# Performance work log

Measured on AMD Instinct MI355X. Metric: run time of the kernel, lower is better.

Reference implementation:

```python
import jax, jax.numpy as jnp
import numpy as np

BEAM = 10; MAX_LEN = 32; PAD = 1; BOS = 2; EOS = 3
NEG = jnp.float32(-1e30)


def lstm_cell(x, h, c, Wih, Whh, bih, bhh):
    # PyTorch LSTMCell gate order: i, f, g, o
    gates = x @ Wih.T + bih + h @ Whh.T + bhh
    i, f, g, o = jnp.split(gates, 4, axis=-1)
    c2 = jax.nn.sigmoid(f) * c + jax.nn.sigmoid(i) * jnp.tanh(g)
    h2 = jax.nn.sigmoid(o) * jnp.tanh(c2)
    return h2, c2


def setup_inputs() -> dict:
    key = jax.random.key(0)
    ks = jax.random.split(key, 14)
    G, P, E, H, S = 1000, 50000, 500, 500, 32
    s = lambda k, shape: jax.random.normal(k, shape, jnp.float32) * 0.05
    return {
        "g_seq": jax.random.randint(ks[0], (S, 1), 0, G),
        "enc_emb": s(ks[1], (G, E)),
        "enc_Wih": s(ks[2], (4 * H, E)), "enc_Whh": s(ks[3], (4 * H, H)),
        "enc_bih": s(ks[4], (4 * H,)), "enc_bhh": s(ks[5], (4 * H,)),
        "dec_emb": s(ks[6], (P, E)),
        "dec_Wih": s(ks[7], (4 * H, E)), "dec_Whh": s(ks[8], (4 * H, H)),
        "dec_bih": s(ks[9], (4 * H,)), "dec_bhh": s(ks[10], (4 * H,)),
        "attn_W": s(ks[11], (H, 2 * H)),
        "out_W": s(ks[12], (P, H)),
        "out_b": s(ks[13], (P,)),
    }


def reference(g_seq, enc_emb, enc_Wih, enc_Whh, enc_bih, enc_bhh,
              dec_emb, dec_Wih, dec_Whh, dec_bih, dec_bhh,
              attn_W, out_W, out_b):
    S = g_seq.shape[0]
    H = enc_Whh.shape[1]
    P = out_W.shape[0]

    # ---- encoder: unidirectional LSTMCell over seq, batch = 1 ----
    e_seq = enc_emb[g_seq[:, 0]]  # (S, E)
    def enc_step(carry, e):
        h, c = carry
        h, c = lstm_cell(e[None, :], h, c, enc_Wih, enc_Whh, enc_bih, enc_bhh)
        return (h, c), h[0]
    h0 = jnp.zeros((1, H), jnp.float32)
    (h, c), outs = jax.lax.scan(enc_step, (h0, h0), e_seq)  # outs: (S, H)

    # expand encoder state / context to beam
    context = jnp.broadcast_to(outs[None, :, :], (BEAM, S, H))
    h = jnp.broadcast_to(h, (BEAM, H))
    c = jnp.broadcast_to(c, (BEAM, H))
    scores = jnp.zeros((BEAM,), jnp.float32)
    tokens = jnp.full((BEAM,), PAD, jnp.int32).at[0].set(BOS)
    row0 = (jnp.arange(BEAM)[:, None] == 0)  # first-step mask: only beam 0 valid

    # ---- beam-search decode loop (run full max_len; early-eos break omitted,
    #      see notes: with eos=3 it only changes output when eos tops beam 0) ----
    def dec_step(carry, t):
        h, c, scores, tokens = carry
        e = dec_emb[tokens]                                   # (BEAM, E)
        h2, c2 = lstm_cell(e, h, c, dec_Wih, dec_Whh, dec_bih, dec_bhh)
        # dot attention
        attn = jax.nn.softmax(jnp.einsum('bsh,bh->bs', context, h2), axis=1)
        wctx = jnp.einsum('bs,bsh->bh', attn, context)
        o = jnp.tanh(jnp.concatenate([h2, wctx], axis=1) @ attn_W.T)
        logp = jax.nn.log_softmax(o @ out_W.T + out_b, axis=1)  # (BEAM, P)
        # first step: only beam 0 participates (original uses workd_lk[0])
        beam_lk = jnp.where(t == 0,
                            jnp.where(row0, logp, NEG),
                            logp + scores[:, None])
        best, idx = jax.lax.top_k(beam_lk.reshape(-1), BEAM)
        prev_k = idx // P
        next_y = idx - prev_k * P
        return (h2[prev_k], c2[prev_k], best, next_y), (prev_k, next_y)

    (_, _, scores, _), (prevKs, nextYs) = jax.lax.scan(
        dec_step, (h, c, scores, tokens), jnp.arange(MAX_LEN))

    # ---- hypothesis traceback, vectorized over beams ----
    def tb_step(k, t):
        tok = nextYs[t][k]
        return prevKs[t][k], tok
    _, toks = jax.lax.scan(tb_step, jnp.arange(BEAM), jnp.arange(MAX_LEN - 1, -1, -1))
    hyps = toks[::-1].T  # (BEAM, MAX_LEN)
    return hyps
```

## Files before the change

kernel.cpp:

```cpp
#include <hip/hip_runtime.h>
#include <math.h>

#define BEAM   10
#define MAXLEN 32
#define SLEN   32
#define HD     500
#define ED     500
#define G4     2000
#define PV     50000
#define NEGF   (-1e30f)

#define OFF_X      0
#define OFF_CBUF   64000
#define OFF_GBUF   65000
#define OFF_CTX    69000
#define OFF_DH     85000
#define OFF_DC     90000
#define OFF_DG     95000
#define OFF_H2     115000
#define OFF_C2     120000
#define OFF_O      130000
#define OFF_SCD    135000
#define OFF_TOK    135020
#define OFF_PREVK  135040
#define OFF_NEXTY  135360
#define OFF_PARTD  136000
#define OFF_CAND   152000
#define OFF_LOG    160000
#define OFF_OWT    660000
#define NEED_T_BYTES ((size_t)(OFF_OWT + (size_t)HD * PV) * 4)

typedef unsigned long long u64;

__device__ __forceinline__ float sigf(float x) { return 1.f / (1.f + expf(-x)); }

__device__ __forceinline__ unsigned fkey(float f) {
    unsigned u = __float_as_uint(f);
    return (u & 0x80000000u) ? ~u : (u | 0x80000000u);
}
__device__ __forceinline__ float unfkey(unsigned k) {
    unsigned u = (k & 0x80000000u) ? (k & 0x7fffffffu) : ~k;
    return __uint_as_float(u);
}

__global__ void k_prep(const int* __restrict__ g_seq, const float* __restrict__ enc_emb,
                       const float* __restrict__ Wih, const float* __restrict__ bih,
                       const float* __restrict__ bhh, float* __restrict__ X,
                       float* __restrict__ cbuf0) {
    if (blockIdx.x == 0) {
        for (int j = threadIdx.x; j < HD; j += 256) cbuf0[j] = 0.f;
    }
    int wv = (blockIdx.x * blockDim.x + threadIdx.x) >> 6;
    int lane = threadIdx.x & 63;
    if (wv >= SLEN * G4) return;
    int t = wv / G4, r = wv - t * G4;
    const float* emb = enc_emb + (size_t)g_seq[t] * ED;
    const float* w = Wih + (size_t)r * ED;
    float acc = 0.f;
    for (int ki = 0; ki < 8; ki++) { int k = ki * 64 + lane; if (k < ED) acc += emb[k] * w[k]; }
    for (int o = 32; o; o >>= 1) acc += __shfl_down(acc, o);
    if (lane == 0) X[t * G4 + r] = acc + bih[r] + bhh[r];
}

__global__ void k_transpose4(const float* __restrict__ outW, float* __restrict__ outW4) {
    __shared__ float t_lds[64][65];
    int tid = threadIdx.x;
    int pbase = blockIdx.x * 64, kbase = blockIdx.y * 64;
    for (int e = 0; e < 16; e++) {
        int idx = e * 256 + tid; int pl = idx >> 6, kl = idx & 63;
        int pp = pbase + pl, kk = kbase + kl;
        t_lds[pl][kl] = (pp < PV && kk < HD) ? outW[(size_t)pp * HD + kk] : 0.f;
    }
    __syncthreads();
    for (int e = 0; e < 4; e++) {
        int idx = e * 256 + tid;
        int pl = idx & 63, kb = idx >> 6;
        int pp = pbase + pl;
        int kglob = kbase + kb * 4;
        if (pp < PV && kglob < HD) {
            float4 v;
            v.x = t_lds[pl][kb * 4 + 0];
            v.y = t_lds[pl][kb * 4 + 1];
            v.z = t_lds[pl][kb * 4 + 2];
            v.w = t_lds[pl][kb * 4 + 3];
            *(float4*)(outW4 + ((size_t)(kbase / 4 + kb) * PV + pp) * 4) = v;
        }
    }
}

__global__ void k_enc(const float* __restrict__ Whh, const float* __restrict__ X,
                      float* __restrict__ gbuf, float* __restrict__ cbuf,
                      float* __restrict__ context, float* __restrict__ dec_h,
                      float* __restrict__ dec_c, double* __restrict__ scores,
                      int* __restrict__ tokens, int t) {
    __shared__ float h_lds[HD];
    const float* gprev = gbuf + ((t + 1) & 1) * G4;
    float*       gcur  = gbuf + (t & 1) * G4;
    const float* cprev = cbuf + ((t + 1) & 1) * HD;
    float*       ccur  = cbuf + (t & 1) * HD;
    int tid = threadIdx.x;
    if (t > 0) {
        for (int j = tid; j < HD; j += 256) {
            float gi = gprev[j], gf = gprev[HD + j], gg = gprev[2 * HD + j], go = gprev[3 * HD + j];
            float c = sigf(gf) * cprev[j] + sigf(gi) * tanhf(gg);
            float h = sigf(go) * tanhf(c);
            h_lds[j] = h;
            if (blockIdx.x == 0) {
                ccur[j] = c;
                context[(t - 1) * HD + j] = h;
                if (t == SLEN) {
                    for (int b = 0; b < BEAM; b++) { dec_h[b * HD + j] = h; dec_c[b * HD + j] = c; }
                }
            }
        }
    } else {
        for (int j = tid; j < HD; j += 256) h_lds[j] = 0.f;
    }
    if (t == SLEN && blockIdx.x == 0 && tid == 0) {
        for (int b = 0; b < BEAM; b++) scores[b] = 0.0;
        tokens[0] = 2; for (int b = 1; b < BEAM; b++) tokens[b] = 1;
    }
    __syncthreads();
    if (t < SLEN) {
        int wv = blockIdx.x * 4 + (tid >> 6), lane = tid & 63;
        for (int r = wv; r < G4; r += 1000) {
            const float* w = Whh + (size_t)r * HD;
            float acc = 0.f;
            for (int ki = 0; ki < 8; ki++) { int k = ki * 64 + lane; if (k < HD) acc += h_lds[k] * w[k]; }
            for (int o = 32; o; o >>= 1) acc += __shfl_down(acc, o);
            if (lane == 0) gcur[r] = X[t * G4 + r] + acc;
        }
    }
}

__global__ __launch_bounds__(1024) void k_gates(
        const float* __restrict__ dec_emb, const float* __restrict__ Wih,
        const float* __restrict__ Whh, const float* __restrict__ bih,
        const float* __restrict__ bhh, const int* __restrict__ tokens,
        const float* __restrict__ h_ws, float* __restrict__ gates) {
    __shared__ float e_lds[BEAM * ED];
    __shared__ float h_lds[BEAM * HD];
    int tid = threadIdx.x;
    for (int idx = tid; idx < BEAM * ED; idx += 1024) {
        int b = idx / ED, k = idx - b * ED;
        e_lds[idx] = dec_emb[(size_t)tokens[b] * ED + k];
        h_lds[idx] = h_ws[idx];
    }
    __syncthreads();
    int wv = tid >> 6, lane = tid & 63;
    int r = blockIdx.x * 16 + wv;
    const float* wi = Wih + (size_t)r * ED;
    const float* wh = Whh + (size_t)r * HD;
    float acc[BEAM];
#pragma unroll
    for (int b = 0; b < BEAM; b++) acc[b] = 0.f;
    for (int ki = 0; ki < 8; ki++) {
        int k = ki * 64 + lane;
        if (k < ED) {
            float w = wi[k];
#pragma unroll
            for (int b = 0; b < BEAM; b++) acc[b] += w * e_lds[b * ED + k];
        }
    }
    for (int ki = 0; ki < 8; ki++) {
        int k = ki * 64 + lane;
        if (k < HD) {
            float w = wh[k];
#pragma unroll
            for (int b = 0; b < BEAM; b++) acc[b] += w * h_lds[b * HD + k];
        }
    }
#pragma unroll
    for (int b = 0; b < BEAM; b++) {
        float v = acc[b];
        for (int o = 32; o; o >>= 1) v += __shfl_down(v, o);
        acc[b] = v;
    }
    if (lane == 0) {
        float bb = bih[r] + bhh[r];
#pragma unroll
        for (int b = 0; b < BEAM; b++) gates[b * G4 + r] = acc[b] + bb;
    }
}

__global__ __launch_bounds__(256) void k_attn_oproj(
        const float* __restrict__ gates, const float* __restrict__ c_ws,
        const float* __restrict__ context, const float* __restrict__ attnW,
        float* __restrict__ h2_ws, float* __restrict__ c2_ws, float* __restrict__ o_ws) {
    __shared__ float h2_lds[BEAM * HD];
    __shared__ float wctx_lds[BEAM * HD];
    __shared__ float s_lds[BEAM * SLEN];
    __shared__ float a_lds[BEAM * SLEN];
    int tid = threadIdx.x;
    int wv = tid >> 6, lane = tid & 63;
    for (int idx = tid; idx < BEAM * HD; idx += 256) {
        int b = idx / HD, j = idx - b * HD;
        float gi = gates[b * G4 + j], gf = gates[b * G4 + HD + j];
        float gg = gates[b * G4 + 2 * HD + j], go = gates[b * G4 + 3 * HD + j];
        float c = sigf(gf) * c_ws[idx] + sigf(gi) * tanhf(gg);
        float h2 = sigf(go) * tanhf(c);
        h2_lds[idx] = h2;
        if (blockIdx.x == 0) { c2_ws[idx] = c; h2_ws[idx] = h2; }
    }
    __syncthreads();
    for (int si = 0; si < 8; ++si) {
        int s = wv + 4 * si;
        float acc[BEAM];
#pragma unroll
        for (int b = 0; b < BEAM; b++) acc[b] = 0.f;
        for (int ki = 0; ki < 8; ki++) {
            int k = ki * 64 + lane;
            if (k < HD) {
                float c = context[s * HD + k];
#pragma unroll
                for (int b = 0; b < BEAM; b++) acc[b] += c * h2_lds[b * HD + k];
            }
        }
#pragma unroll
        for (int b = 0; b < BEAM; b++) {
            float v = acc[b];
            for (int o = 32; o; o >>= 1) v += __shfl_down(v, o);
            if (lane == 0) s_lds[b * SLEN + s] = v;
        }
    }
    __syncthreads();
    if (wv == 0) {
        for (int b = 0; b < BEAM; ++b) {
            float v = (lane < SLEN) ? s_lds[b * SLEN + lane] : -INFINITY;
            float m = v;
            for (int o = 32; o; o >>= 1) m = fmaxf(m, __shfl_xor(m, o));
            float e = (lane < SLEN) ? expf(v - m) : 0.f;
            float sum = e;
            for (int o = 32; o; o >>= 1) sum += __shfl_xor(sum, o);
            if (lane < SLEN) a_lds[b * SLEN + lane] = e / sum;
        }
    }
    __syncthreads();
    {
        float w0[BEAM], w1[BEAM];
#pragma unroll
        for (int b = 0; b < BEAM; b++) { w0[b] = 0.f; w1[b] = 0.f; }
        int j0 = tid, j1 = tid + 256;
        for (int s = 0; s < SLEN; ++s) {
            float c0 = (j0 < HD) ? context[s * HD + j0] : 0.f;
            float c1 = (j1 < HD) ? context[s * HD + j1] : 0.f;
#pragma unroll
            for (int b = 0; b < BEAM; b++) {
                float a = a_lds[b * SLEN + s];
                w0[b] += a * c0; w1[b] += a * c1;
            }
        }
#pragma unroll
        for (int b = 0; b < BEAM; b++) {
            if (j0 < HD) wctx_lds[b * HD + j0] = w0[b];
            if (j1 < HD) wctx_lds[b * HD + j1] = w1[b];
        }
    }
    __syncthreads();
    int j = blockIdx.x * 4 + wv;
    const float* w = attnW + (size_t)j * 1000;
    float acc[BEAM];
#pragma unroll
    for (int b = 0; b < BEAM; b++) acc[b] = 0.f;
    for (int ki = 0; ki < 16; ki++) {
        int k = ki * 64 + lane;
        if (k < 1000) {
            float wk = w[k];
#pragma unroll
            for (int b = 0; b < BEAM; b++) {
                float h = (k < HD) ? h2_lds[b * HD + k] : wctx_lds[b * HD + k - HD];
                acc[b] += wk * h;
            }
        }
    }
#pragma unroll
    for (int b = 0; b < BEAM; b++) {
        float v = acc[b];
        for (int o = 32; o; o >>= 1) v += __shfl_down(v, o);
        acc[b] = v;
    }
    if (lane == 0) {
#pragma unroll
        for (int b = 0; b < BEAM; b++) o_ws[b * HD + j] = tanhf(acc[b]);
    }
}

__global__ __launch_bounds__(256) void k_logits4(
        const float* __restrict__ outW4, const float* __restrict__ outB,
        const float* __restrict__ o_ws, float* __restrict__ logits,
        double* __restrict__ partials) {
    __shared__ __align__(16) float4 o4[BEAM * 125];
    __shared__ float part[4][64][BEAM];
    int tid = threadIdx.x;
    for (int idx = tid; idx < BEAM * 125; idx += 256) {
        int b = idx / 125, kb = idx - b * 125;
        o4[idx] = *(const float4*)(o_ws + b * HD + kb * 4);
    }
    __syncthreads();
    int kc = tid >> 6, pl = tid & 63;
    int p = blockIdx.x * 64 + pl;
    int pc = (p < PV) ? p : (PV - 1);
    int kb0 = kc * 32, kb1 = (kc == 3) ? 125 : (kb0 + 32);
    float acc[BEAM];
#pragma unroll
    for (int b = 0; b < BEAM; b++) acc[b] = 0.f;
    const float4* wp = (const float4*)outW4;
    for (int kb = kb0; kb < kb1; ++kb) {
        float4 w = wp[(size_t)kb * PV + pc];
#pragma unroll
        for (int b = 0; b < BEAM; b++) {
            float4 o = o4[b * 125 + kb];
            acc[b] += w.x * o.x + w.y * o.y + w.z * o.z + w.w * o.w;
        }
    }
#pragma unroll
    for (int b = 0; b < BEAM; b++) part[kc][pl][b] = acc[b];
    __syncthreads();
    if (tid < 64) {
        int p2 = blockIdx.x * 64 + tid;
        bool valid = (p2 < PV);
        float ob = outB[valid ? p2 : 0];
        double es[BEAM];
#pragma unroll
        for (int b = 0; b < BEAM; b++) {
            float lg = part[0][tid][b] + part[1][tid][b] + part[2][tid][b] + part[3][tid][b] + ob;
            if (valid) logits[(size_t)b * PV + p2] = lg;
            es[b] = valid ? exp((double)lg) : 0.0;
        }
#pragma unroll
        for (int b = 0; b < BEAM; b++) {
            for (int o = 32; o; o >>= 1) es[b] += __shfl_down(es[b], o);
        }
        if (tid == 0) {
#pragma unroll
            for (int b = 0; b < BEAM; b++) partials[blockIdx.x * BEAM + b] = es[b];
        }
    }
}

__global__ void k_logits_f(const float* __restrict__ outW, const float* __restrict__ outB,
                           const float* __restrict__ o_ws, float* __restrict__ logits,
                           double* __restrict__ partials) {
    __shared__ float o_lds[BEAM * HD];
    __shared__ double ered[4][BEAM];
    int tid = threadIdx.x;
    for (int idx = tid; idx < BEAM * HD; idx += 256) o_lds[idx] = o_ws[idx];
    __syncthreads();
    int wv = tid >> 6, lane = tid & 63;
    int w = blockIdx.x * 4 + wv;
    double esum = 0.0;
    for (int pi = 0; pi < 16; pi++) {
        int p = w * 16 + pi;
        if (p >= PV) break;
        const float* wr = outW + (size_t)p * HD;
        float acc[BEAM];
#pragma unroll
        for (int b = 0; b < BEAM; b++) acc[b] = 0.f;
        for (int ki = 0; ki < 8; ki++) {
            int k = ki * 64 + lane;
            if (k < HD) {
                float x = wr[k];
#pragma unroll
                for (int b = 0; b < BEAM; b++) acc[b] += x * o_lds[b * HD + k];
            }
        }
#pragma unroll
        for (int b = 0; b < BEAM; b++)
            for (int o = 32; o; o >>= 1) acc[b] += __shfl_xor(acc[b], o);
        if (lane < BEAM) {
            float lg = 0.f;
#pragma unroll
            for (int b = 0; b < BEAM; b++) if (lane == b) lg = acc[b];
            lg += outB[p];
            logits[(size_t)lane * PV + p] = lg;
            esum += exp((double)lg);
        }
    }
    if (lane < BEAM) ered[wv][lane] = esum;
    __syncthreads();
    if (tid < BEAM) partials[blockIdx.x * BEAM + tid] =
        ered[0][tid] + ered[1][tid] + ered[2][tid] + ered[3][tid];
}

__global__ __launch_bounds__(256) void k_topk_row(const float* __restrict__ logits,
                                                  u64* __restrict__ cands) {
    const int CH = 1563;
    int r = blockIdx.x >> 5, ci = blockIdx.x & 31;
    int base = ci * CH;
    int tid = threadIdx.x;
    int wv = tid >> 6, lane = tid & 63;
    u64 key[7];
#pragma unroll
    for (int e = 0; e < 7; e++) {
        int p = base + e * 256 + tid;
        key[e] = 0ull;
        if (p < base + CH && p < PV) {
            float v = logits[(size_t)r * PV + p];
            key[e] = ((u64)fkey(v) << 32) | (unsigned)(~(unsigned)p);
        }
    }
    __shared__ u64 wred[4];
    __shared__ u64 winlds;
    for (int round = 0; round < BEAM; round++) {
        u64 mx = 0ull;
#pragma unroll
        for (int e = 0; e < 7; e++) if (key[e] > mx) mx = key[e];
        for (int o = 32; o; o >>= 1) {
            u64 other = __shfl_down(mx, o);
            if (other > mx) mx = other;
        }
        if (lane == 0) wred[wv] = mx;
        __syncthreads();
        if (tid == 0) {
            u64 wn = wred[0];
            for (int i = 1; i < 4; i++) if (wred[i] > wn) wn = wred[i];
            winlds = wn;
            cands[blockIdx.x * BEAM + round] = wn;
        }
        __syncthreads();
        u64 win = winlds;
#pragma unroll
        for (int e = 0; e < 7; e++) if (key[e] == win) key[e] = 0ull;
    }
}

__global__ __launch_bounds__(256) void k_merge(
        const double* __restrict__ partials, int npart,
        const u64* __restrict__ cands,
        double* __restrict__ scores, int* __restrict__ tokens,
        const float* __restrict__ h2_ws, const float* __restrict__ c2_ws,
        float* __restrict__ h_ws, float* __restrict__ c_ws,
        int* __restrict__ prevKs, int* __restrict__ nextYs, int t) {
    __shared__ double wredd[4];
    __shared__ double lse_lds[BEAM];
    __shared__ double sc_lds[BEAM];
    __shared__ double bwv[4];
    __shared__ unsigned bwf[4];
    __shared__ double winv_s;
    __shared__ unsigned winf_s;
    __shared__ int pk_lds[BEAM];
    __shared__ int ny_lds[BEAM];
    __shared__ double val_lds[BEAM];
    int tid = threadIdx.x;
    int wv = tid >> 6, lane = tid & 63;
    if (tid < BEAM) sc_lds[tid] = scores[tid];
    for (int b = 0; b < BEAM; b++) {
        double s = 0.0;
        for (int j = tid; j < npart; j += 256) s += partials[j * BEAM + b];
        for (int o = 32; o; o >>= 1) s += __shfl_down(s, o);
        if (lane == 0) wredd[wv] = s;
        __syncthreads();
        if (tid == 0) lse_lds[b] = log(wredd[0] + wredd[1] + wredd[2] + wredd[3]);
        __syncthreads();
    }
    double   cv[13];
    unsigned cf[13];
#pragma unroll
    for (int e = 0; e < 13; e++) {
        int c = e * 256 + tid;
        cv[e] = -1.0e308; cf[e] = 0xFFFFFFFFu;
        if (c < 3200) {
            u64 k0 = cands[c];
            if (k0) {
                int r = c / 320;
                float v = unfkey((unsigned)(k0 >> 32));
                unsigned p = ~((unsigned)k0);
                double v2;
                if (t == 0) v2 = (r == 0) ? ((double)v - lse_lds[0]) : (double)NEGF;
                else        v2 = ((double)v - lse_lds[r]) + sc_lds[r];
                cv[e] = v2;
                cf[e] = (unsigned)r * PV + p;
            }
        }
    }
    for (int round = 0; round < BEAM; round++) {
        double bv = -1.0e308; unsigned bf = 0xFFFFFFFFu;
#pragma unroll
        for (int e = 0; e < 13; e++) {
            if (cv[e] > bv || (cv[e] == bv && cf[e] < bf)) { bv = cv[e]; bf = cf[e]; }
        }
        for (int o = 32; o; o >>= 1) {
            double ov = __shfl_down(bv, o);
            unsigned of = __shfl_down(bf, o);
            if (ov > bv || (ov == bv && of < bf)) { bv = ov; bf = of; }
        }
        if (lane == 0) { bwv[wv] = bv; bwf[wv] = bf; }
        __syncthreads();
        if (tid == 0) {
            double xv = bwv[0]; unsigned xf = bwf[0];
            for (int i = 1; i < 4; i++) {
                if (bwv[i] > xv || (bwv[i] == xv && bwf[i] < xf)) { xv = bwv[i]; xf = bwf[i]; }
            }
            winv_s = xv; winf_s = xf;
            int pk = (int)(xf / PV);
            int ny = (int)(xf - (unsigned)pk * PV);
            pk_lds[round] = pk; ny_lds[round] = ny; val_lds[round] = xv;
        }
        __syncthreads();
        unsigned wff = winf_s;
#pragma unroll
        for (int e = 0; e < 13; e++) {
            if (cf[e] == wff) { cv[e] = -1.0e308; cf[e] = 0xFFFFFFFFu; }
        }
    }
    if (tid < BEAM) {
        scores[tid] = val_lds[tid];
        tokens[tid] = ny_lds[tid];
        prevKs[t * BEAM + tid] = pk_lds[tid];
        nextYs[t * BEAM + tid] = ny_lds[tid];
    }
    __syncthreads();
    for (int idx = tid; idx < BEAM * HD; idx += 256) {
        int i = idx / HD, j = idx - i * HD;
        h_ws[idx] = h2_ws[pk_lds[i] * HD + j];
        c_ws[idx] = c2_ws[pk_lds[i] * HD + j];
    }
}

__global__ void k_traceback(const int* __restrict__ prevKs, const int* __restrict__ nextYs,
                            int* __restrict__ out) {
    int k = threadIdx.x;
    if (k >= BEAM) return;
    int cur = k;
    for (int t = MAXLEN - 1; t >= 0; t--) {
        out[k * MAXLEN + t] = nextYs[t * BEAM + cur];
        cur = prevKs[t * BEAM + cur];
    }
}

extern "C" void kernel_launch(void* const* d_in, const int* in_sizes, int n_in,
                              void* d_out, int out_size, void* d_ws, size_t ws_size,
                              hipStream_t stream) {
    const int*   g_seq  = (const int*)  d_in[0];
    const float* encEmb = (const float*)d_in[1];
    const float* encWih = (const float*)d_in[2];
    const float* encWhh = (const float*)d_in[3];
    const float* encBih = (const float*)d_in[4];
    const float* encBhh = (const float*)d_in[5];
    const float* decEmb = (const float*)d_in[6];
    const float* decWih = (const float*)d_in[7];
    const float* decWhh = (const float*)d_in[8];
    const float* decBih = (const float*)d_in[9];
    const float* decBhh = (const float*)d_in[10];
    const float* attnW  = (const float*)d_in[11];
    const float* outW   = (const float*)d_in[12];
    const float* outB   = (const float*)d_in[13];

    float* ws = (float*)d_ws;
    float*  X     = ws + OFF_X;
    float*  cbuf  = ws + OFF_CBUF;
    float*  gbuf  = ws + OFF_GBUF;
    float*  ctx   = ws + OFF_CTX;
    float*  dh    = ws + OFF_DH;
    float*  dc    = ws + OFF_DC;
    float*  dg    = ws + OFF_DG;
    float*  h2    = ws + OFF_H2;
    float*  c2    = ws + OFF_C2;
    float*  o     = ws + OFF_O;
    double* sc    = (double*)(ws + OFF_SCD);
    int*    tok   = (int*)(ws + OFF_TOK);
    int*    prevK = (int*)(ws + OFF_PREVK);
    int*    nextY = (int*)(ws + OFF_NEXTY);
    double* part  = (double*)(ws + OFF_PARTD);
    u64*    cand  = (u64*)(ws + OFF_CAND);
    float*  logits = ws + OFF_LOG;
    float*  outW4  = ws + OFF_OWT;

    bool bigws = (ws_size >= NEED_T_BYTES);

    k_prep<<<16000, 256, 0, stream>>>(g_seq, encEmb, encWih, encBih, encBhh, X, cbuf);
    if (bigws) k_transpose4<<<dim3(782, 8), 256, 0, stream>>>(outW, outW4);

    for (int t = 0; t <= SLEN; t++)
        k_enc<<<250, 256, 0, stream>>>(encWhh, X, gbuf, cbuf, ctx, dh, dc, sc, tok, t);

    const int npart = 782;
    for (int t = 0; t < MAXLEN; t++) {
        k_gates<<<125, 1024, 0, stream>>>(decEmb, decWih, decWhh, decBih, decBhh, tok, dh, dg);
        k_attn_oproj<<<125, 256, 0, stream>>>(dg, dc, ctx, attnW, h2, c2, o);
        if (bigws) k_logits4<<<782, 256, 0, stream>>>(outW4, outB, o, logits, part);
        else       k_logits_f<<<782, 256, 0, stream>>>(outW, outB, o, logits, part);
        k_topk_row<<<320, 256, 0, stream>>>(logits, cand);
        k_merge<<<1, 256, 0, stream>>>(part, npart, cand, sc, tok, h2, c2, dh, dc, prevK, nextY, t);
    }
    k_traceback<<<1, 64, 0, stream>>>(prevK, nextY, (int*)d_out);
}
```

Before: 4.218 ms.

## Fuse encoder and beam-search decode loop into one cooperative persistent kernel

New measurement: 4.217 ms. No clear change (-0.0%).

```diff
diff --git a/kernel.cpp b/kernel.cpp
--- a/kernel.cpp
+++ b/kernel.cpp
@@ -1,5 +1,8 @@
 #include <hip/hip_runtime.h>
+#include <hip/hip_cooperative_groups.h>
 #include <math.h>
+
+namespace cg = cooperative_groups;
 
 #define BEAM   10
 #define MAXLEN 32
@@ -9,6 +12,13 @@
 #define G4     2000
 #define PV     50000
 #define NEGF   (-1e30f)
+
+#define GRID   256
+#define NW     1024
+
+#define NCHUNK 25
+#define CHSZ   2000
+#define CANDN  (NCHUNK * BEAM * BEAM)
 
 #define OFF_X      0
 #define OFF_CBUF   64000
@@ -84,6 +94,445 @@
             v.z = t_lds[pl][kb * 4 + 2];
             v.w = t_lds[pl][kb * 4 + 3];
             *(float4*)(outW4 + ((size_t)(kbase / 4 + kb) * PV + pp) * 4) = v;
+        }
+    }
+}
+
+struct MegaA {
+    const float* encWhh; const float* X;
+    float* gbuf; float* cbuf; float* ctx;
+    const float* decEmb; const float* decWih; const float* decWhh;
+    const float* decBih; const float* decBhh; const float* attnW;
+    const float* outW4; const float* outW; const float* outB;
+    float* dh; float* dc; float* dg; float* h2w; float* c2w; float* ow;
+    float* logits; double* sc; double* part;
+    int* tok; int* prevK; int* nextY; u64* cand; int* outTok;
+    int bigws; int npart;
+};
+
+struct TopkSm { u64 wred[4]; u64 win; };
+struct MergeSm {
+    double wredd[4];
+    double lse[BEAM];
+    double scl[BEAM];
+    double bwv[4];
+    unsigned bwf[4];
+    unsigned winf;
+    int pk[BEAM]; int ny[BEAM];
+    double val[BEAM];
+};
+
+__global__ __launch_bounds__(256) void k_mega(MegaA A) {
+    __shared__ __align__(16) char smem_raw[43584];
+    float* smf = (float*)smem_raw;
+    cg::grid_group grid = cg::this_grid();
+    const int tid = threadIdx.x, bid = blockIdx.x;
+    const int wv = tid >> 6, lane = tid & 63;
+    const int gw = bid * 4 + wv;
+
+    for (int t = 0; t <= SLEN; ++t) {
+        const float* gprev = A.gbuf + ((t + 1) & 1) * G4;
+        float*       gcur  = A.gbuf + (t & 1) * G4;
+        const float* cprev = A.cbuf + ((t + 1) & 1) * HD;
+        float*       ccur  = A.cbuf + (t & 1) * HD;
+        bool par = (t < SLEN) || (bid == 0);
+        if (par) {
+            float* h_lds = smf;
+            if (t > 0) {
+                for (int j = tid; j < HD; j += 256) {
+                    float gi = gprev[j], gf = gprev[HD + j], gg = gprev[2 * HD + j], go = gprev[3 * HD + j];
+                    float c = sigf(gf) * cprev[j] + sigf(gi) * tanhf(gg);
+                    float h = sigf(go) * tanhf(c);
+                    h_lds[j] = h;
+                    if (bid == 0) {
+                        ccur[j] = c;
+                        A.ctx[(t - 1) * HD + j] = h;
+                        if (t == SLEN) {
+                            for (int b = 0; b < BEAM; b++) { A.dh[b * HD + j] = h; A.dc[b * HD + j] = c; }
+                        }
+                    }
+                }
+            } else {
+                for (int j = tid; j < HD; j += 256) h_lds[j] = 0.f;
+            }
+            if (t == SLEN && bid == 0 && tid == 0) {
+                for (int b = 0; b < BEAM; b++) A.sc[b] = 0.0;
+                A.tok[0] = 2; for (int b = 1; b < BEAM; b++) A.tok[b] = 1;
+            }
+            __syncthreads();
+            if (t < SLEN) {
+                for (int r = gw; r < G4; r += NW) {
+                    const float* w = A.encWhh + (size_t)r * HD;
+                    float acc = 0.f;
+                    for (int ki = 0; ki < 8; ki++) { int k = ki * 64 + lane; if (k < HD) acc += h_lds[k] * w[k]; }
+                    for (int o = 32; o; o >>= 1) acc += __shfl_down(acc, o);
+                    if (lane == 0) gcur[r] = A.X[t * G4 + r] + acc;
+                }
+            }
+        }
+        grid.sync();
+    }
+
+    for (int t = 0; t < MAXLEN; ++t) {
+        {
+            float* e_lds = smf;
+            float* h_lds = smf + BEAM * ED;
+            for (int idx = tid; idx < BEAM * ED; idx += 256) {
+                int b = idx / ED, k = idx - b * ED;
+                e_lds[idx] = A.decEmb[(size_t)A.tok[b] * ED + k];
+                h_lds[idx] = A.dh[idx];
+            }
+            __syncthreads();
+            for (int r = gw; r < G4; r += NW) {
+                const float* wi = A.decWih + (size_t)r * ED;
+                const float* wh = A.decWhh + (size_t)r * HD;
+                float acc[BEAM];
+#pragma unroll
+                for (int b = 0; b < BEAM; b++) acc[b] = 0.f;
+                for (int ki = 0; ki < 8; ki++) {
+                    int k = ki * 64 + lane;
+                    if (k < ED) {
+                        float w = wi[k];
+#pragma unroll
+                        for (int b = 0; b < BEAM; b++) acc[b] += w * e_lds[b * ED + k];
+                    }
+                }
+                for (int ki = 0; ki < 8; ki++) {
+                    int k = ki * 64 + lane;
+                    if (k < HD) {
+                        float w = wh[k];
+#pragma unroll
+                        for (int b = 0; b < BEAM; b++) acc[b] += w * h_lds[b * HD + k];
+                    }
+                }
+#pragma unroll
+                for (int b = 0; b < BEAM; b++) {
+                    float v = acc[b];
+                    for (int o = 32; o; o >>= 1) v += __shfl_down(v, o);
+                    acc[b] = v;
+                }
+                if (lane == 0) {
+                    float bb = A.decBih[r] + A.decBhh[r];
+#pragma unroll
+                    for (int b = 0; b < BEAM; b++) A.dg[b * G4 + r] = acc[b] + bb;
+                }
+            }
+        }
+        grid.sync();
+
+        if (bid < 125) {
+            float* h2_lds   = smf;
+            float* wctx_lds = smf + 5000;
+            float* s_lds    = smf + 10000;
+            float* a_lds    = smf + 10320;
+            for (int idx = tid; idx < BEAM * HD; idx += 256) {
+                int b = idx / HD, j = idx - b * HD;
+                float gi = A.dg[b * G4 + j], gf = A.dg[b * G4 + HD + j];
+                float gg = A.dg[b * G4 + 2 * HD + j], go = A.dg[b * G4 + 3 * HD + j];
+                float c = sigf(gf) * A.dc[idx] + sigf(gi) * tanhf(gg);
+                float h2 = sigf(go) * tanhf(c);
+                h2_lds[idx] = h2;
+                if (bid == 0) { A.c2w[idx] = c; A.h2w[idx] = h2; }
+            }
+            __syncthreads();
+            for (int si = 0; si < 8; ++si) {
+                int s = wv + 4 * si;
+                float acc[BEAM];
+#pragma unroll
+                for (int b = 0; b < BEAM; b++) acc[b] = 0.f;
+                for (int ki = 0; ki < 8; ki++) {
+                    int k = ki * 64 + lane;
+                    if (k < HD) {
+                        float c = A.ctx[s * HD + k];
+#pragma unroll
+                        for (int b = 0; b < BEAM; b++) acc[b] += c * h2_lds[b * HD + k];
+                    }
+                }
+#pragma unroll
+                for (int b = 0; b < BEAM; b++) {
+                    float v = acc[b];
+                    for (int o = 32; o; o >>= 1) v += __shfl_down(v, o);
+                    if (lane == 0) s_lds[b * SLEN + s] = v;
+                }
+            }
+            __syncthreads();
+            if (wv == 0) {
+                for (int b = 0; b < BEAM; ++b) {
+                    float v = (lane < SLEN) ? s_lds[b * SLEN + lane] : -INFINITY;
+                    float m = v;
+                    for (int o = 32; o; o >>= 1) m = fmaxf(m, __shfl_xor(m, o));
+                    float e = (lane < SLEN) ? expf(v - m) : 0.f;
+                    float sum = e;
+                    for (int o = 32; o; o >>= 1) sum += __shfl_xor(sum, o);
+                    if (lane < SLEN) a_lds[b * SLEN + lane] = e / sum;
+                }
+            }
+            __syncthreads();
+            {
+                float w0[BEAM], w1[BEAM];
+#pragma unroll
+                for (int b = 0; b < BEAM; b++) { w0[b] = 0.f; w1[b] = 0.f; }
+                int j0 = tid, j1 = tid + 256;
+                for (int s = 0; s < SLEN; ++s) {
+                    float c0 = (j0 < HD) ? A.ctx[s * HD + j0] : 0.f;
+                    float c1 = (j1 < HD) ? A.ctx[s * HD + j1] : 0.f;
+#pragma unroll
+                    for (int b = 0; b < BEAM; b++) {
+                        float a = a_lds[b * SLEN + s];
+                        w0[b] += a * c0; w1[b] += a * c1;
+                    }
+                }
+#pragma unroll
+                for (int b = 0; b < BEAM; b++) {
+                    if (j0 < HD) wctx_lds[b * HD + j0] = w0[b];
+                    if (j1 < HD) wctx_lds[b * HD + j1] = w1[b];
+                }
+            }
+            __syncthreads();
+            int j = gw;
+            const float* w = A.attnW + (size_t)j * 1000;
+            float acc[BEAM];
+#pragma unroll
+            for (int b = 0; b < BEAM; b++) acc[b] = 0.f;
+            for (int ki = 0; ki < 16; ki++) {
+                int k = ki * 64 + lane;
+                if (k < 1000) {
+                    float wk = w[k];
+#pragma unroll
+                    for (int b = 0; b < BEAM; b++) {
+                        float h = (k < HD) ? h2_lds[b * HD + k] : wctx_lds[b * HD + k - HD];
+                        acc[b] += wk * h;
+                    }
+                }
+            }
+#pragma unroll
+            for (int b = 0; b < BEAM; b++) {
+                float v = acc[b];
+                for (int o = 32; o; o >>= 1) v += __shfl_down(v, o);
+                acc[b] = v;
+            }
+            if (lane == 0) {
+#pragma unroll
+                for (int b = 0; b < BEAM; b++) A.ow[b * HD + j] = tanhf(acc[b]);
+            }
+        }
+        grid.sync();
+
+        {
+            float4* o4 = (float4*)smem_raw;
+            for (int idx = tid; idx < BEAM * 125; idx += 256) {
+                int b = idx / 125, kb = idx - b * 125;
+                o4[idx] = *(const float4*)(A.ow + b * HD + kb * 4);
+            }
+            __syncthreads();
+            if (A.bigws) {
+                float* partl = (float*)(smem_raw + 20032);
+                for (int pt = bid; pt < 782; pt += GRID) {
+                    int kc = tid >> 6, pl = tid & 63;
+                    int p = pt * 64 + pl;
+                    int pc = (p < PV) ? p : (PV - 1);
+                    int kb0 = kc * 32, kb1 = (kc == 3) ? 125 : (kb0 + 32);
+                    float acc[BEAM];
+#pragma unroll
+                    for (int b = 0; b < BEAM; b++) acc[b] = 0.f;
+                    const float4* wp = (const float4*)A.outW4;
+                    for (int kb = kb0; kb < kb1; ++kb) {
+                        float4 w = wp[(size_t)kb * PV + pc];
+#pragma unroll
+                        for (int b = 0; b < BEAM; b++) {
+                            float4 o = o4[b * 125 + kb];
+                            acc[b] += w.x * o.x + w.y * o.y + w.z * o.z + w.w * o.w;
+                        }
+                    }
+#pragma unroll
+                    for (int b = 0; b < BEAM; b++) partl[(kc * 64 + pl) * BEAM + b] = acc[b];
+                    __syncthreads();
+                    if (tid < 64) {
+                        int p2 = pt * 64 + tid;
+                        bool valid = (p2 < PV);
+                        float ob = A.outB[valid ? p2 : 0];
+                        double es[BEAM];
+#pragma unroll
+                        for (int b = 0; b < BEAM; b++) {
+                            float lg = partl[(0 * 64 + tid) * BEAM + b] + partl[(1 * 64 + tid) * BEAM + b]
+                                     + partl[(2 * 64 + tid) * BEAM + b] + partl[(3 * 64 + tid) * BEAM + b] + ob;
+                            if (valid) A.logits[(size_t)b * PV + p2] = lg;
+                            es[b] = valid ? exp((double)lg) : 0.0;
+                        }
+#pragma unroll
+                        for (int b = 0; b < BEAM; b++) {
+                            for (int o = 32; o; o >>= 1) es[b] += __shfl_down(es[b], o);
+                        }
+                        if (tid == 0) {
+#pragma unroll
+                            for (int b = 0; b < BEAM; b++) A.part[pt * BEAM + b] = es[b];
+                        }
+                    }
+                    __syncthreads();
+                }
+            } else {
+                float* o_lds = (float*)smem_raw;
+                double* ered = (double*)(smem_raw + 20032);
+                double esum = 0.0;
+                for (int w = gw; w * 16 < PV; w += NW) {
+                    for (int pi = 0; pi < 16; pi++) {
+                        int p = w * 16 + pi;
+                        if (p >= PV) break;
+                        const float* wr = A.outW + (size_t)p * HD;
+                        float acc[BEAM];
+#pragma unroll
+                        for (int b = 0; b < BEAM; b++) acc[b] = 0.f;
+                        for (int ki = 0; ki < 8; ki++) {
+                            int k = ki * 64 + lane;
+                            if (k < HD) {
+                                float x = wr[k];
+#pragma unroll
+                                for (int b = 0; b < BEAM; b++) acc[b] += x * o_lds[b * HD + k];
+                            }
+                        }
+#pragma unroll
+                        for (int b = 0; b < BEAM; b++)
+                            for (int o = 32; o; o >>= 1) acc[b] += __shfl_xor(acc[b], o);
+                        if (lane < BEAM) {
+                            float lg = 0.f;
+#pragma unroll
+                            for (int b = 0; b < BEAM; b++) if (lane == b) lg = acc[b];
+                            lg += A.outB[p];
+                            A.logits[(size_t)lane * PV + p] = lg;
+                            esum += exp((double)lg);
+                        }
+                    }
+                }
+                if (lane < BEAM) ered[wv * BEAM + lane] = esum;
+                __syncthreads();
+                if (tid < BEAM)
+                    A.part[bid * BEAM + tid] = ered[0 * BEAM + tid] + ered[1 * BEAM + tid]
+                                             + ered[2 * BEAM + tid] + ered[3 * BEAM + tid];
+            }
+        }
+        grid.sync();
+
+        if (bid < NCHUNK * BEAM) {
+            TopkSm* T = (TopkSm*)smem_raw;
+            int r = bid / NCHUNK, ci = bid - r * NCHUNK;
+            int base = ci * CHSZ;
+            u64 key[8];
+#pragma unroll
+            for (int e = 0; e < 8; e++) {
+                int p = base + e * 256 + tid;
+                key[e] = 0ull;
+                if (p < base + CHSZ && p < PV) {
+                    float v = A.logits[(size_t)r * PV + p];
+                    key[e] = ((u64)fkey(v) << 32) | (unsigned)(~(unsigned)p);
+                }
+            }
+            for (int round = 0; round < BEAM; round++) {
+                u64 mx = 0ull;
+#pragma unroll
+                for (int e = 0; e < 8; e++) if (key[e] > mx) mx = key[e];
+                for (int o = 32; o; o >>= 1) {
+                    u64 other = __shfl_down(mx, o);
+                    if (other > mx) mx = other;
+                }
+                if (lane == 0) T->wred[wv] = mx;
+                __syncthreads();
+                if (tid == 0) {
+                    u64 wn = T->wred[0];
+                    for (int i = 1; i < 4; i++) if (T->wred[i] > wn) wn = T->wred[i];
+                    T->win = wn;
+                    A.cand[bid * BEAM + round] = wn;
+                }
+                __syncthreads();
+                u64 win = T->win;
+#pragma unroll
+                for (int e = 0; e < 8; e++) if (key[e] == win) key[e] = 0ull;
+            }
+        }
+        grid.sync();
+
+        if (bid == 0) {
+            MergeSm* M = (MergeSm*)smem_raw;
+            if (tid < BEAM) M->scl[tid] = A.sc[tid];
+            for (int b = 0; b < BEAM; b++) {
+                double s = 0.0;
+                for (int j = tid; j < A.npart; j += 256) s += A.part[j * BEAM + b];
+                for (int o = 32; o; o >>= 1) s += __shfl_down(s, o);
+                if (lane == 0) M->wredd[wv] = s;
+                __syncthreads();
+                if (tid == 0) M->lse[b] = log(M->wredd[0] + M->wredd[1] + M->wredd[2] + M->wredd[3]);
+                __syncthreads();
+            }
+            double   cv[10];
+            unsigned cf[10];
+#pragma unroll
+            for (int e = 0; e < 10; e++) {
+                int c = e * 256 + tid;
+                cv[e] = -1.0e308; cf[e] = 0xFFFFFFFFu;
+                if (c < CANDN) {
+                    u64 k0 = A.cand[c];
+                    if (k0) {
+                        int r = c / (NCHUNK * BEAM);
+                        float v = unfkey((unsigned)(k0 >> 32));
+                        unsigned p = ~((unsigned)k0);
+                        double v2;
+                        if (t == 0) v2 = (r == 0) ? ((double)v - M->lse[0]) : (double)NEGF;
+                        else        v2 = ((double)v - M->lse[r]) + M->scl[r];
+                        cv[e] = v2;
+                        cf[e] = (unsigned)r * PV + p;
+                    }
+                }
+            }
+            for (int round = 0; round < BEAM; round++) {
+                double bv = -1.0e308; unsigned bf = 0xFFFFFFFFu;
+#pragma unroll
+                for (int e = 0; e < 10; e++) {
+                    if (cv[e] > bv || (cv[e] == bv && cf[e] < bf)) { bv = cv[e]; bf = cf[e]; }
+                }
+                for (int o = 32; o; o >>= 1) {
+                    double ov = __shfl_down(bv, o);
+                    unsigned of = __shfl_down(bf, o);
+                    if (ov > bv || (ov == bv && of < bf)) { bv = ov; bf = of; }
+                }
+                if (lane == 0) { M->bwv[wv] = bv; M->bwf[wv] = bf; }
+                __syncthreads();
+                if (tid == 0) {
+                    double xv = M->bwv[0]; unsigned xf = M->bwf[0];
+                    for (int i = 1; i < 4; i++) {
+                        if (M->bwv[i] > xv || (M->bwv[i] == xv && M->bwf[i] < xf)) { xv = M->bwv[i]; xf = M->bwf[i]; }
+                    }
+                    M->winf = xf;
+                    int pk = (int)(xf / PV);
+                    int ny = (int)(xf - (unsigned)pk * PV);
+                    M->pk[round] = pk; M->ny[round] = ny; M->val[round] = xv;
+                }
+                __syncthreads();
+                unsigned wff = M->winf;
+#pragma unroll
+                for (int e = 0; e < 10; e++) {
+                    if (cf[e] == wff) { cv[e] = -1.0e308; cf[e] = 0xFFFFFFFFu; }
+                }
+            }
+            if (tid < BEAM) {
+                A.sc[tid] = M->val[tid];
+                A.tok[tid] = M->ny[tid];
+                A.prevK[t * BEAM + tid] = M->pk[tid];
+                A.nextY[t * BEAM + tid] = M->ny[tid];
+            }
+            __syncthreads();
+            for (int idx = tid; idx < BEAM * HD; idx += 256) {
+                int i = idx / HD, j = idx - i * HD;
+                A.dh[idx] = A.h2w[M->pk[i] * HD + j];
+                A.dc[idx] = A.c2w[M->pk[i] * HD + j];
+            }
+        }
+        grid.sync();
+    }
+
+    if (bid == 0 && tid < BEAM) {
+        int cur = tid;
+        for (int tt = MAXLEN - 1; tt >= 0; tt--) {
+            A.outTok[tid * MAXLEN + tt] = A.nextY[tt * BEAM + cur];
+            cur = A.prevK[tt * BEAM + cur];
         }
     }
 }
@@ -436,7 +885,6 @@
     __shared__ double sc_lds[BEAM];
     __shared__ double bwv[4];
     __shared__ unsigned bwf[4];
-    __shared__ double winv_s;
     __shared__ unsigned winf_s;
     __shared__ int pk_lds[BEAM];
     __shared__ int ny_lds[BEAM];
@@ -491,7 +939,7 @@
             for (int i = 1; i < 4; i++) {
                 if (bwv[i] > xv || (bwv[i] == xv && bwf[i] < xf)) { xv = bwv[i]; xf = bwf[i]; }
             }
-            winv_s = xv; winf_s = xf;
+            winf_s = xf;
             int pk = (int)(xf / PV);
             int ny = (int)(xf - (unsigned)pk * PV);
             pk_lds[round] = pk; ny_lds[round] = ny; val_lds[round] = xv;
@@ -571,17 +1019,51 @@
     k_prep<<<16000, 256, 0, stream>>>(g_seq, encEmb, encWih, encBih, encBhh, X, cbuf);
     if (bigws) k_transpose4<<<dim3(782, 8), 256, 0, stream>>>(outW, outW4);
 
-    for (int t = 0; t <= SLEN; t++)
-        k_enc<<<250, 256, 0, stream>>>(encWhh, X, gbuf, cbuf, ctx, dh, dc, sc, tok, t);
-
-    const int npart = 782;
-    for (int t = 0; t < MAXLEN; t++) {
-        k_gates<<<125, 1024, 0, stream>>>(decEmb, decWih, decWhh, decBih, decBhh, tok, dh, dg);
-        k_attn_oproj<<<125, 256, 0, stream>>>(dg, dc, ctx, attnW, h2, c2, o);
-        if (bigws) k_logits4<<<782, 256, 0, stream>>>(outW4, outB, o, logits, part);
-        else       k_logits_f<<<782, 256, 0, stream>>>(outW, outB, o, logits, part);
-        k_topk_row<<<320, 256, 0, stream>>>(logits, cand);
-        k_merge<<<1, 256, 0, stream>>>(part, npart, cand, sc, tok, h2, c2, dh, dc, prevK, nextY, t);
-    }
-    k_traceback<<<1, 64, 0, stream>>>(prevK, nextY, (int*)d_out);
-}
+    bool coop_ok = false;
+    {
+        int dev = 0;
+        if (hipGetDevice(&dev) == hipSuccess) {
+            hipDeviceProp_t prop;
+            if (hipGetDeviceProperties(&prop, dev) == hipSuccess && prop.cooperativeLaunch) {
+                int occ = 0;
+                if (hipOccupancyMaxActiveBlocksPerMultiprocessor(&occ, (const void*)k_mega, 256, 0)
+                        == hipSuccess) {
+                    if ((long long)occ * prop.multiProcessorCount >= GRID) coop_ok = true;
+                }
+            }
+        }
+    }
+
+    hipError_t err = hipErrorUnknown;
+    if (coop_ok) {
+        MegaA a;
+        a.encWhh = encWhh; a.X = X;
+        a.gbuf = gbuf; a.cbuf = cbuf; a.ctx = ctx;
+        a.decEmb = decEmb; a.decWih = decWih; a.decWhh = decWhh;
+        a.decBih = decBih; a.decBhh = decBhh; a.attnW = attnW;
+        a.outW4 = outW4; a.outW = outW; a.outB = outB;
+        a.dh = dh; a.dc = dc; a.dg = dg; a.h2w = h2; a.c2w = c2; a.ow = o;
+        a.logits = logits; a.sc = sc; a.part = part;
+        a.tok = tok; a.prevK = prevK; a.nextY = nextY; a.cand = cand;
+        a.outTok = (int*)d_out;
+        a.bigws = bigws ? 1 : 0;
+        a.npart = bigws ? 782 : GRID;
+        void* params[] = { (void*)&a };
+        err = hipLaunchCooperativeKernel((const void*)k_mega, dim3(GRID), dim3(256),
+                                         params, 0, stream);
+    }
+    if (err != hipSuccess) {
+        for (int t = 0; t <= SLEN; t++)
+            k_enc<<<250, 256, 0, stream>>>(encWhh, X, gbuf, cbuf, ctx, dh, dc, sc, tok, t);
+        const int npart = 782;
+        for (int t = 0; t < MAXLEN; t++) {
+            k_gates<<<125, 1024, 0, stream>>>(decEmb, decWih, decWhh, decBih, decBhh, tok, dh, dg);
+            k_attn_oproj<<<125, 256, 0, stream>>>(dg, dc, ctx, attnW, h2, c2, o);
+            if (bigws) k_logits4<<<782, 256, 0, stream>>>(outW4, outB, o, logits, part);
+            else       k_logits_f<<<782, 256, 0, stream>>>(outW, outB, o, logits, part);
+            k_topk_row<<<320, 256, 0, stream>>>(logits, cand);
+            k_merge<<<1, 256, 0, stream>>>(part, npart, cand, sc, tok, h2, c2, dh, dc, prevK, nextY, t);
+        }
+        k_traceback<<<1, 64, 0, stream>>>(prevK, nextY, (int*)d_out);
+    }
+}
```
